# Kernel optimization log

Hardware: AMD Instinct MI355X
Metric: run time of the kernel (lower is better)

The kernel has to match this reference:

```python
import jax, jax.numpy as jnp
import numpy as np

NUM_GRAPHS = 64


def setup_inputs() -> dict:
    key = jax.random.key(0)
    ks = jax.random.split(key, 8)
    N, E, D_IN, D_H = 50000, 800000, 128, 256
    x = jax.random.uniform(ks[0], (N, D_IN), dtype=jnp.float32)
    edge_index = jax.random.randint(ks[1], (2, E), 0, N, dtype=jnp.int64)
    batch = jnp.sort(jax.random.randint(ks[2], (N,), 0, NUM_GRAPHS, dtype=jnp.int64))
    s = 1.0 / np.sqrt(D_IN)
    s2 = 1.0 / np.sqrt(D_H)
    W1_rel = jax.random.normal(ks[3], (D_IN, D_H), dtype=jnp.float32) * s
    W1_root = jax.random.normal(ks[4], (D_IN, D_H), dtype=jnp.float32) * s
    b1 = jnp.zeros((D_H,), jnp.float32)
    W2_rel = jax.random.normal(ks[5], (D_H, D_H), dtype=jnp.float32) * s2
    W2_root = jax.random.normal(ks[6], (D_H, D_H), dtype=jnp.float32) * s2
    b2 = jnp.zeros((D_H,), jnp.float32)
    return {"x": x, "edge_index": edge_index, "batch": batch,
            "W1_rel": W1_rel, "W1_root": W1_root, "b1": b1,
            "W2_rel": W2_rel, "W2_root": W2_root, "b2": b2}


def reference(x, edge_index, batch, W1_rel, W1_root, b1, W2_rel, W2_root, b2):
    N = x.shape[0]
    src, dst = edge_index[0], edge_index[1]

    # handcrafted features: per-label fraction of total feature mass + log(graph_size)
    graph_size = jnp.sum(x)
    handcrafted = jnp.concatenate([jnp.sum(x, axis=0) / graph_size,
                                   jnp.log(graph_size)[None]])

    def graph_conv(h, W_rel, W_root, b):
        # PyG GraphConv (aggr='add'): out_i = W_rel @ sum_{j->i} h_j + W_root @ h_i + b
        agg = jax.ops.segment_sum(h[src], dst, num_segments=N)  # [N, d]
        return agg @ W_rel + h @ W_root + b

    h = jax.nn.relu(graph_conv(x, W1_rel, W1_root, b1))
    # layers 2..num_layers share the same weights (module instance reused in original)
    for _ in range(2):
        h = jax.nn.relu(graph_conv(h, W2_rel, W2_root, b2))

    # global_mean_pool over batch ids
    counts = jax.ops.segment_sum(jnp.ones((N,), h.dtype), batch, num_segments=NUM_GRAPHS)
    pooled = jax.ops.segment_sum(h, batch, num_segments=NUM_GRAPHS)
    pooled = pooled / jnp.maximum(counts, 1.0)[:, None]
    return pooled, handcrafted
```

## Files before the change

kernel.cpp:

```cpp
#include <hip/hip_runtime.h>
#include <hip/hip_bf16.h>
#include <string.h>

#define NN 50000
#define NE 800000
#define DIN 128
#define DH 256
#define NG 64
#define PSPLIT 32

typedef short bf16x8 __attribute__((ext_vector_type(8)));
typedef float f32x4 __attribute__((ext_vector_type(4)));

__device__ __forceinline__ float bf2f(__hip_bfloat16 v) { return __bfloat162float(v); }
__device__ __forceinline__ float bfbits(unsigned int lo16) {
  unsigned int u = lo16 << 16;
  float f;
  memcpy(&f, &u, 4);
  return f;
}
__device__ __forceinline__ unsigned int packbf2(float x, float y) {
  __hip_bfloat16 bx = __float2bfloat16(x), by = __float2bfloat16(y);
  unsigned short ux, uy;
  memcpy(&ux, &bx, 2);
  memcpy(&uy, &by, 2);
  return (unsigned int)ux | ((unsigned int)uy << 16);
}

__device__ __forceinline__ float loadF(const void* p, long i, int fbf) {
  return fbf ? bf2f(((const __hip_bfloat16*)p)[i]) : ((const float*)p)[i];
}
__device__ __forceinline__ void storeF(void* p, long i, float v, int fbf) {
  if (fbf) ((__hip_bfloat16*)p)[i] = __float2bfloat16(v);
  else ((float*)p)[i] = v;
}
__device__ __forceinline__ int loadI(const void* p, long i, int i64) {
  return i64 ? (int)((const long long*)p)[i] : ((const int*)p)[i];
}

__global__ void k_detect(const void* x, const void* ei, int* flags) {
  __shared__ int s_f32sig, s_i32sig;
  if (threadIdx.x == 0) { s_f32sig = 0; s_i32sig = 0; }
  __syncthreads();
  int t = threadIdx.x;
  const unsigned short* u = (const unsigned short*)x;
  int f = 0;
  for (int i = 2 * t; i < 8192; i += 512) if (u[i] >= 0x4000) f = 1;
  const unsigned int* w = (const unsigned int*)ei;
  int g = 0;
  for (int i = 2 * t + 1; i < 8192; i += 512) if (w[i] != 0u) g = 1;
  if (f) atomicOr(&s_f32sig, 1);
  if (g) atomicOr(&s_i32sig, 1);
  __syncthreads();
  if (t == 0) { flags[0] = s_f32sig ? 0 : 1; flags[1] = s_i32sig ? 0 : 1; }
}

__global__ void k_zero(int* __restrict__ p, int n) {
  int i = blockIdx.x * blockDim.x + threadIdx.x;
  int stride = gridDim.x * blockDim.x;
  for (; i < n; i += stride) p[i] = 0;
}

__global__ __launch_bounds__(256) void k_prep(
    const void* __restrict__ x, __hip_bfloat16* __restrict__ xb,
    float* __restrict__ colsum, const int* __restrict__ flags) {
  int fbf = flags[0];
  int t = threadIdx.x;
  int lane16 = t & 15;
  int rowoff = t >> 4;
  float acc[8] = {};
  for (int r = blockIdx.x * 16 + rowoff; r < NN; r += gridDim.x * 16) {
    uint4 o;
    if (fbf) {
      uint4 v = ((const uint4*)x)[(long)r * 16 + lane16];
      acc[0] += bfbits(v.x & 0xffffu); acc[1] += bfbits(v.x >> 16);
      acc[2] += bfbits(v.y & 0xffffu); acc[3] += bfbits(v.y >> 16);
      acc[4] += bfbits(v.z & 0xffffu); acc[5] += bfbits(v.z >> 16);
      acc[6] += bfbits(v.w & 0xffffu); acc[7] += bfbits(v.w >> 16);
      o = v;
    } else {
      float4 a = ((const float4*)x)[(long)r * 32 + lane16 * 2];
      float4 b = ((const float4*)x)[(long)r * 32 + lane16 * 2 + 1];
      acc[0] += a.x; acc[1] += a.y; acc[2] += a.z; acc[3] += a.w;
      acc[4] += b.x; acc[5] += b.y; acc[6] += b.z; acc[7] += b.w;
      o.x = packbf2(a.x, a.y); o.y = packbf2(a.z, a.w);
      o.z = packbf2(b.x, b.y); o.w = packbf2(b.z, b.w);
    }
    ((uint4*)xb)[(long)r * 16 + lane16] = o;
  }
  __shared__ float s[16][DIN];
#pragma unroll
  for (int k = 0; k < 8; ++k) s[rowoff][lane16 * 8 + k] = acc[k];
  __syncthreads();
  if (t < DIN) {
    float v = 0.f;
#pragma unroll
    for (int ro = 0; ro < 16; ++ro) v += s[ro][t];
    atomicAdd(&colsum[t], v);
  }
}

__global__ void k_handcrafted(const float* __restrict__ colsum, void* __restrict__ out,
                              const int* __restrict__ flags) {
  __shared__ float s[DIN];
  int fbf = flags[0];
  int t = threadIdx.x;
  s[t] = colsum[t];
  __syncthreads();
  for (int off = DIN / 2; off > 0; off >>= 1) {
    if (t < off) s[t] += s[t + off];
    __syncthreads();
  }
  float g = s[0];
  storeF(out, NG * DH + t, colsum[t] / g, fbf);
  if (t == 0) storeF(out, NG * DH + DIN, logf(g), fbf);
}

__global__ void k_pack_w(const void* __restrict__ Wrel, const void* __restrict__ Wroot,
                         const void* __restrict__ bias, __hip_bfloat16* __restrict__ pack,
                         float* __restrict__ biasf, const int* __restrict__ flags, int K) {
  int fbf = flags[0];
  int KS = K >> 5;
  int total = 2 * K * DH;
  int i = blockIdx.x * blockDim.x + threadIdx.x;
  int stride = gridDim.x * blockDim.x;
  for (int p = i; p < total; p += stride) {
    int m = p / (K * DH);
    int r = p % (K * DH);
    int j = r & 7;
    int l = (r >> 3) & 63;
    int q2 = r >> 9;
    int ks = q2 % KS;
    int ct = q2 / KS;
    int kk = ks * 32 + (l >> 4) * 8 + j;
    int col = ct * 16 + (l & 15);
    const void* W = m ? Wroot : Wrel;
    pack[p] = __float2bfloat16(loadF(W, (long)kk * DH + col, fbf));
  }
  if (i < DH) biasf[i] = loadF(bias, i, fbf);
}

__global__ void k_deg(const void* __restrict__ ei, int* __restrict__ cnt,
                      const int* __restrict__ flags) {
  int i64 = flags[1];
  int e = blockIdx.x * blockDim.x + threadIdx.x;
  int stride = gridDim.x * blockDim.x;
  for (; e < NE; e += stride) {
    int d = loadI(ei, (long)NE + e, i64);
    d = min(max(d, 0), NN - 1);
    atomicAdd(&cnt[d], 1);
  }
}

#define SCAN_B 256
__global__ void k_scan1(const int* __restrict__ cnt, int* __restrict__ rowptr,
                        int* __restrict__ bsum) {
  __shared__ int s[SCAN_B];
  int b = blockIdx.x, t = threadIdx.x;
  int i = b * SCAN_B + t;
  int v = (i < NN) ? cnt[i] : 0;
  s[t] = v;
  __syncthreads();
  for (int off = 1; off < SCAN_B; off <<= 1) {
    int xv = (t >= off) ? s[t - off] : 0;
    __syncthreads();
    s[t] += xv;
    __syncthreads();
  }
  if (i < NN) rowptr[i] = s[t] - v;
  if (t == SCAN_B - 1) bsum[b] = s[t];
}

__global__ void k_scan2(int* __restrict__ bsum, int nb) {
  __shared__ int s[SCAN_B];
  int t = threadIdx.x;
  int v = (t < nb) ? bsum[t] : 0;
  s[t] = v;
  __syncthreads();
  for (int off = 1; off < SCAN_B; off <<= 1) {
    int xv = (t >= off) ? s[t - off] : 0;
    __syncthreads();
    s[t] += xv;
    __syncthreads();
  }
  if (t < nb) bsum[t] = s[t] - v;
}

__global__ void k_scan3(int* __restrict__ rowptr, const int* __restrict__ bsum) {
  int i = blockIdx.x * blockDim.x + threadIdx.x;
  int stride = gridDim.x * blockDim.x;
  for (; i < NN; i += stride) rowptr[i] += bsum[i >> 8];
  if (blockIdx.x == 0 && threadIdx.x == 0) rowptr[NN] = NE;
}

__global__ void k_fill(const void* __restrict__ ei, const int* __restrict__ rowptr,
                       int* __restrict__ cur, int* __restrict__ srcs,
                       const int* __restrict__ flags) {
  int i64 = flags[1];
  int e = blockIdx.x * blockDim.x + threadIdx.x;
  int stride = gridDim.x * blockDim.x;
  for (; e < NE; e += stride) {
    int s = loadI(ei, e, i64);
    int d = loadI(ei, (long)NE + e, i64);
    s = min(max(s, 0), NN - 1);
    d = min(max(d, 0), NN - 1);
    int p = atomicAdd(&cur[d], 1);
    srcs[rowptr[d] + p] = s;
  }
}

__global__ __launch_bounds__(256) void k_gather256(
    const int* __restrict__ rowptr, const int* __restrict__ srcs,
    const __hip_bfloat16* __restrict__ h, __hip_bfloat16* __restrict__ agg) {
  int node = blockIdx.x * 4 + (threadIdx.x >> 6);
  if (node >= NN) return;
  int lane = threadIdx.x & 63;
  int beg = rowptr[node], end = rowptr[node + 1];
  const uint2* h2 = (const uint2*)h;
  float a0 = 0.f, a1 = 0.f, a2 = 0.f, a3 = 0.f;
  int i = beg;
  for (; i + 7 < end; i += 8) {
    uint2 v[8];
#pragma unroll
    for (int u = 0; u < 8; ++u) v[u] = h2[srcs[i + u] * 64 + lane];
#pragma unroll
    for (int u = 0; u < 8; ++u) {
      a0 += bfbits(v[u].x & 0xffffu);
      a1 += bfbits(v[u].x >> 16);
      a2 += bfbits(v[u].y & 0xffffu);
      a3 += bfbits(v[u].y >> 16);
    }
  }
  for (; i < end; ++i) {
    uint2 v0 = h2[srcs[i] * 64 + lane];
    a0 += bfbits(v0.x & 0xffffu);
    a1 += bfbits(v0.x >> 16);
    a2 += bfbits(v0.y & 0xffffu);
    a3 += bfbits(v0.y >> 16);
  }
  uint2 o;
  o.x = packbf2(a0, a1);
  o.y = packbf2(a2, a3);
  ((uint2*)agg)[node * 64 + lane] = o;
}

__global__ __launch_bounds__(256) void k_gather128(
    const int* __restrict__ rowptr, const int* __restrict__ srcs,
    const __hip_bfloat16* __restrict__ h, __hip_bfloat16* __restrict__ agg) {
  int node = blockIdx.x * 4 + (threadIdx.x >> 6);
  if (node >= NN) return;
  int lane = threadIdx.x & 63;
  int beg = rowptr[node], end = rowptr[node + 1];
  const unsigned int* h2 = (const unsigned int*)h;
  float a0 = 0.f, a1 = 0.f;
  int i = beg;
  for (; i + 7 < end; i += 8) {
    unsigned int v[8];
#pragma unroll
    for (int u = 0; u < 8; ++u) v[u] = h2[srcs[i + u] * 64 + lane];
#pragma unroll
    for (int u = 0; u < 8; ++u) {
      a0 += bfbits(v[u] & 0xffffu);
      a1 += bfbits(v[u] >> 16);
    }
  }
  for (; i < end; ++i) {
    unsigned int v0 = h2[srcs[i] * 64 + lane];
    a0 += bfbits(v0 & 0xffffu);
    a1 += bfbits(v0 >> 16);
  }
  ((unsigned int*)agg)[node * 64 + lane] = packbf2(a0, a1);
}

template <int K>
__global__ __launch_bounds__(256, 4) void k_gemm(
    const __hip_bfloat16* __restrict__ A1, const __hip_bfloat16* __restrict__ A2,
    const __hip_bfloat16* __restrict__ Wpack, const float* __restrict__ bias,
    __hip_bfloat16* __restrict__ out) {
  constexpr int KS = K >> 5;
  int lane = threadIdx.x & 63;
  int wave = threadIdx.x >> 6;
  int m15 = lane & 15;
  int q = lane >> 4;
  int row0 = blockIdx.x * 32;
  const short* A1s = (const short*)A1;
  const short* A2s = (const short*)A2;
  const short* Wp = (const short*)Wpack;
  const int wrootOfs = K * DH;
  f32x4 acc[2][4] = {};
#pragma unroll
  for (int ks = 0; ks < KS; ++ks) {
    int kofs = ks * 32 + q * 8;
    bf16x8 a1[2], a2[2], b1[4], b2[4];
#pragma unroll
    for (int mt = 0; mt < 2; ++mt) {
      int r = row0 + mt * 16 + m15;
      if (r > NN - 1) r = NN - 1;
      a1[mt] = *(const bf16x8*)(A1s + r * K + kofs);
      a2[mt] = *(const bf16x8*)(A2s + r * K + kofs);
    }
#pragma unroll
    for (int ct = 0; ct < 4; ++ct) {
      int gct = wave * 4 + ct;
      const short* base = Wp + ((gct * KS + ks) * 64 + lane) * 8;
      b1[ct] = *(const bf16x8*)(base);
      b2[ct] = *(const bf16x8*)(base + wrootOfs);
    }
#pragma unroll
    for (int mt = 0; mt < 2; ++mt)
#pragma unroll
      for (int ct = 0; ct < 4; ++ct) {
        acc[mt][ct] = __builtin_amdgcn_mfma_f32_16x16x32_bf16(a1[mt], b1[ct], acc[mt][ct], 0, 0, 0);
        acc[mt][ct] = __builtin_amdgcn_mfma_f32_16x16x32_bf16(a2[mt], b2[ct], acc[mt][ct], 0, 0, 0);
      }
  }
#pragma unroll
  for (int mt = 0; mt < 2; ++mt)
#pragma unroll
    for (int ct = 0; ct < 4; ++ct) {
      int col = (wave * 4 + ct) * 16 + m15;
      float bv = bias[col];
#pragma unroll
      for (int r = 0; r < 4; ++r) {
        int row = row0 + mt * 16 + q * 4 + r;
        if (row < NN) {
          float v = acc[mt][ct][r] + bv;
          out[row * DH + col] = __float2bfloat16(fmaxf(v, 0.f));
        }
      }
    }
}

__global__ void k_bounds(const void* __restrict__ batch, int* __restrict__ gstart,
                         int* __restrict__ gend, const int* __restrict__ flags) {
  int i64 = flags[1];
  int n = blockIdx.x * blockDim.x + threadIdx.x;
  if (n >= NN) return;
  int b = min(max(loadI(batch, n, i64), 0), NG - 1);
  int bp = (n == 0) ? -1 : min(max(loadI(batch, n - 1, i64), 0), NG - 1);
  if (b != bp) gstart[b] = n;
  int bn = (n == NN - 1) ? -1 : min(max(loadI(batch, n + 1, i64), 0), NG - 1);
  if (b != bn) gend[b] = n + 1;
}

__global__ void k_poolpart(const int* __restrict__ gstart, const int* __restrict__ gend,
                           const __hip_bfloat16* __restrict__ h, float* __restrict__ pooled) {
  int g = blockIdx.x;
  int p = blockIdx.y;
  int j = threadIdx.x;
  int s = gstart[g], e = gend[g];
  int len = e - s;
  if (len <= 0) return;
  int chunk = (len + PSPLIT - 1) / PSPLIT;
  int rs = s + p * chunk;
  int re = min(rs + chunk, e);
  if (rs >= re) return;
  const unsigned int* h2 = (const unsigned int*)h;
  float a0 = 0.f, a1 = 0.f;
  for (int r = rs; r < re; ++r) {
    unsigned int v = h2[(long)r * 128 + j];
    a0 += bfbits(v & 0xffffu);
    a1 += bfbits(v >> 16);
  }
  atomicAdd(&pooled[g * DH + 2 * j], a0);
  atomicAdd(&pooled[g * DH + 2 * j + 1], a1);
}

__global__ void k_poolfin(const int* __restrict__ gstart, const int* __restrict__ gend,
                          const float* __restrict__ pooled, void* __restrict__ out,
                          const int* __restrict__ flags) {
  int fbf = flags[0];
  int g = blockIdx.x;
  int j = threadIdx.x;
  float cnt = fmaxf((float)(gend[g] - gstart[g]), 1.0f);
  storeF(out, (long)g * DH + j, pooled[g * DH + j] / cnt, fbf);
}

extern "C" void kernel_launch(void* const* d_in, const int* in_sizes, int n_in,
                              void* d_out, int out_size, void* d_ws, size_t ws_size,
                              hipStream_t stream) {
  const void* x = d_in[0];
  const void* ei = d_in[1];
  const void* batch = d_in[2];
  const void* W1r = d_in[3];
  const void* W1o = d_in[4];
  const void* b1 = d_in[5];
  const void* W2r = d_in[6];
  const void* W2o = d_in[7];
  const void* b2 = d_in[8];
  void* out = d_out;

  char* w = (char*)d_ws;
  auto alloc = [&](size_t bytes) -> char* {
    char* p = w;
    w += (bytes + 255) & ~(size_t)255;
    return p;
  };
  int* flags = (int*)alloc(64);
  const int zero_n = NN + NN + DIN + NG + NG + NG * DH;
  int* zreg = (int*)alloc((size_t)zero_n * 4);
  int* cnt = zreg;
  int* cur = cnt + NN;
  float* colsum = (float*)(cur + NN);
  int* gstart = (int*)(colsum + DIN);
  int* gend = gstart + NG;
  float* pooled = (float*)(gend + NG);
  int* rowptr = (int*)alloc((NN + 1) * 4);
  int* bsum = (int*)alloc(SCAN_B * 4);
  int* srcs = (int*)alloc((size_t)NE * 4);
  __hip_bfloat16* xb = (__hip_bfloat16*)alloc((size_t)NN * DIN * 2);
  __hip_bfloat16* aggb = (__hip_bfloat16*)alloc((size_t)NN * DH * 2);
  __hip_bfloat16* hA = (__hip_bfloat16*)alloc((size_t)NN * DH * 2);
  __hip_bfloat16* hB = (__hip_bfloat16*)alloc((size_t)NN * DH * 2);
  __hip_bfloat16* wp1 = (__hip_bfloat16*)alloc((size_t)2 * DIN * DH * 2);
  __hip_bfloat16* wp2 = (__hip_bfloat16*)alloc((size_t)2 * DH * DH * 2);
  float* b1f = (float*)alloc(DH * 4);
  float* b2f = (float*)alloc(DH * 4);

  const int nblk = (NN + SCAN_B - 1) / SCAN_B;
  const int gemm_grid = (NN + 31) / 32;
  const int gat_grid = (NN + 3) / 4;

  k_detect<<<1, 256, 0, stream>>>(x, ei, flags);
  k_zero<<<512, 256, 0, stream>>>(zreg, zero_n);

  k_pack_w<<<64, 256, 0, stream>>>(W1r, W1o, b1, wp1, b1f, flags, DIN);
  k_pack_w<<<128, 256, 0, stream>>>(W2r, W2o, b2, wp2, b2f, flags, DH);
  k_prep<<<1024, 256, 0, stream>>>(x, xb, colsum, flags);
  k_handcrafted<<<1, 128, 0, stream>>>(colsum, out, flags);

  k_deg<<<1024, 256, 0, stream>>>(ei, cnt, flags);
  k_scan1<<<nblk, SCAN_B, 0, stream>>>(cnt, rowptr, bsum);
  k_scan2<<<1, SCAN_B, 0, stream>>>(bsum, nblk);
  k_scan3<<<256, 256, 0, stream>>>(rowptr, bsum);
  k_fill<<<1024, 256, 0, stream>>>(ei, rowptr, cur, srcs, flags);

  k_gather128<<<gat_grid, 256, 0, stream>>>(rowptr, srcs, xb, aggb);
  k_gemm<DIN><<<gemm_grid, 256, 0, stream>>>(aggb, xb, wp1, b1f, hA);
  k_gather256<<<gat_grid, 256, 0, stream>>>(rowptr, srcs, hA, aggb);
  k_gemm<DH><<<gemm_grid, 256, 0, stream>>>(aggb, hA, wp2, b2f, hB);
  k_gather256<<<gat_grid, 256, 0, stream>>>(rowptr, srcs, hB, aggb);
  k_gemm<DH><<<gemm_grid, 256, 0, stream>>>(aggb, hB, wp2, b2f, hA);

  k_bounds<<<nblk, 256, 0, stream>>>(batch, gstart, gend, flags);
  k_poolpart<<<dim3(NG, PSPLIT), 128, 0, stream>>>(gstart, gend, hA, pooled);
  k_poolfin<<<NG, DH, 0, stream>>>(gstart, gend, pooled, out, flags);
}
```

Measured before the change: 499.6 us.

## Split gather kernels into column slices with edge-parallel lanes per node

The neighbor-gather kernels now split the feature columns into 8 slices handled by separate blocks, with block id low bits selecting the slice. Within a wave, lane groups process different edges of the same node in parallel and are combined with shuffle reductions. The aim is a smaller per-pass working set of h that fits better in cache, plus more memory-level parallelism per node. Edge index loads and agg stores use nontemporal hints. In exchange, the srcs lists and rowptr are re-read 8 times and each 4-byte load is narrow and scattered.

```diff
diff --git a/kernel.cpp b/kernel.cpp
--- a/kernel.cpp
+++ b/kernel.cpp
@@ -209,67 +209,93 @@
   }
 }
 
-__global__ __launch_bounds__(256) void k_gather256(
+#define GNB ((NN + 15) / 16)
+
+__global__ __launch_bounds__(256) void k_gather256x(
     const int* __restrict__ rowptr, const int* __restrict__ srcs,
     const __hip_bfloat16* __restrict__ h, __hip_bfloat16* __restrict__ agg) {
-  int node = blockIdx.x * 4 + (threadIdx.x >> 6);
-  if (node >= NN) return;
+  int bid = blockIdx.x;
+  int s = bid & 7;
+  int nb = bid >> 3;
+  int wave = threadIdx.x >> 6;
   int lane = threadIdx.x & 63;
-  int beg = rowptr[node], end = rowptr[node + 1];
-  const uint2* h2 = (const uint2*)h;
-  float a0 = 0.f, a1 = 0.f, a2 = 0.f, a3 = 0.f;
-  int i = beg;
-  for (; i + 7 < end; i += 8) {
-    uint2 v[8];
-#pragma unroll
-    for (int u = 0; u < 8; ++u) v[u] = h2[srcs[i + u] * 64 + lane];
-#pragma unroll
-    for (int u = 0; u < 8; ++u) {
-      a0 += bfbits(v[u].x & 0xffffu);
-      a1 += bfbits(v[u].x >> 16);
-      a2 += bfbits(v[u].y & 0xffffu);
-      a3 += bfbits(v[u].y >> 16);
-    }
-  }
-  for (; i < end; ++i) {
-    uint2 v0 = h2[srcs[i] * 64 + lane];
-    a0 += bfbits(v0.x & 0xffffu);
-    a1 += bfbits(v0.x >> 16);
-    a2 += bfbits(v0.y & 0xffffu);
-    a3 += bfbits(v0.y >> 16);
-  }
-  uint2 o;
-  o.x = packbf2(a0, a1);
-  o.y = packbf2(a2, a3);
-  ((uint2*)agg)[node * 64 + lane] = o;
-}
-
-__global__ __launch_bounds__(256) void k_gather128(
+  int g = lane >> 4;
+  int c = lane & 15;
+  const unsigned int* h2 = (const unsigned int*)h;
+  unsigned int* agg2 = (unsigned int*)agg;
+  int colofs = s * 16 + c;
+#pragma unroll
+  for (int nw = 0; nw < 4; ++nw) {
+    int node = nb * 16 + wave * 4 + nw;
+    if (node >= NN) break;
+    int beg = rowptr[node], end = rowptr[node + 1];
+    float a0 = 0.f, a1 = 0.f;
+    int i = beg + g;
+    for (; i + 12 < end; i += 16) {
+      int s0 = __builtin_nontemporal_load(&srcs[i]);
+      int s1 = __builtin_nontemporal_load(&srcs[i + 4]);
+      int s2 = __builtin_nontemporal_load(&srcs[i + 8]);
+      int s3 = __builtin_nontemporal_load(&srcs[i + 12]);
+      unsigned v0 = h2[(long)s0 * 128 + colofs];
+      unsigned v1 = h2[(long)s1 * 128 + colofs];
+      unsigned v2 = h2[(long)s2 * 128 + colofs];
+      unsigned v3 = h2[(long)s3 * 128 + colofs];
+      a0 += bfbits(v0 & 0xffffu) + bfbits(v1 & 0xffffu) +
+            bfbits(v2 & 0xffffu) + bfbits(v3 & 0xffffu);
+      a1 += bfbits(v0 >> 16) + bfbits(v1 >> 16) + bfbits(v2 >> 16) + bfbits(v3 >> 16);
+    }
+    for (; i < end; i += 4) {
+      int s0 = __builtin_nontemporal_load(&srcs[i]);
+      unsigned v0 = h2[(long)s0 * 128 + colofs];
+      a0 += bfbits(v0 & 0xffffu);
+      a1 += bfbits(v0 >> 16);
+    }
+    a0 += __shfl_xor(a0, 16); a0 += __shfl_xor(a0, 32);
+    a1 += __shfl_xor(a1, 16); a1 += __shfl_xor(a1, 32);
+    if (g == 0)
+      __builtin_nontemporal_store(packbf2(a0, a1), &agg2[(long)node * 128 + colofs]);
+  }
+}
+
+__global__ __launch_bounds__(256) void k_gather128x(
     const int* __restrict__ rowptr, const int* __restrict__ srcs,
     const __hip_bfloat16* __restrict__ h, __hip_bfloat16* __restrict__ agg) {
-  int node = blockIdx.x * 4 + (threadIdx.x >> 6);
-  if (node >= NN) return;
+  int bid = blockIdx.x;
+  int s = bid & 7;
+  int nb = bid >> 3;
+  int wave = threadIdx.x >> 6;
   int lane = threadIdx.x & 63;
-  int beg = rowptr[node], end = rowptr[node + 1];
+  int g = lane >> 3;
+  int c = lane & 7;
   const unsigned int* h2 = (const unsigned int*)h;
-  float a0 = 0.f, a1 = 0.f;
-  int i = beg;
-  for (; i + 7 < end; i += 8) {
-    unsigned int v[8];
-#pragma unroll
-    for (int u = 0; u < 8; ++u) v[u] = h2[srcs[i + u] * 64 + lane];
-#pragma unroll
-    for (int u = 0; u < 8; ++u) {
-      a0 += bfbits(v[u] & 0xffffu);
-      a1 += bfbits(v[u] >> 16);
-    }
-  }
-  for (; i < end; ++i) {
-    unsigned int v0 = h2[srcs[i] * 64 + lane];
-    a0 += bfbits(v0 & 0xffffu);
-    a1 += bfbits(v0 >> 16);
-  }
-  ((unsigned int*)agg)[node * 64 + lane] = packbf2(a0, a1);
+  unsigned int* agg2 = (unsigned int*)agg;
+  int colofs = s * 8 + c;
+#pragma unroll
+  for (int nw = 0; nw < 4; ++nw) {
+    int node = nb * 16 + wave * 4 + nw;
+    if (node >= NN) break;
+    int beg = rowptr[node], end = rowptr[node + 1];
+    float a0 = 0.f, a1 = 0.f;
+    int i = beg + g;
+    for (; i + 8 < end; i += 16) {
+      int s0 = __builtin_nontemporal_load(&srcs[i]);
+      int s1 = __builtin_nontemporal_load(&srcs[i + 8]);
+      unsigned v0 = h2[(long)s0 * 64 + colofs];
+      unsigned v1 = h2[(long)s1 * 64 + colofs];
+      a0 += bfbits(v0 & 0xffffu) + bfbits(v1 & 0xffffu);
+      a1 += bfbits(v0 >> 16) + bfbits(v1 >> 16);
+    }
+    for (; i < end; i += 8) {
+      int s0 = __builtin_nontemporal_load(&srcs[i]);
+      unsigned v0 = h2[(long)s0 * 64 + colofs];
+      a0 += bfbits(v0 & 0xffffu);
+      a1 += bfbits(v0 >> 16);
+    }
+    a0 += __shfl_xor(a0, 8); a0 += __shfl_xor(a0, 16); a0 += __shfl_xor(a0, 32);
+    a1 += __shfl_xor(a1, 8); a1 += __shfl_xor(a1, 16); a1 += __shfl_xor(a1, 32);
+    if (g == 0)
+      __builtin_nontemporal_store(packbf2(a0, a1), &agg2[(long)node * 64 + colofs]);
+  }
 }
 
 template <int K>
@@ -419,7 +445,7 @@
 
   const int nblk = (NN + SCAN_B - 1) / SCAN_B;
   const int gemm_grid = (NN + 31) / 32;
-  const int gat_grid = (NN + 3) / 4;
+  const int gat_grid = 8 * GNB;
 
   k_detect<<<1, 256, 0, stream>>>(x, ei, flags);
   k_zero<<<512, 256, 0, stream>>>(zreg, zero_n);
@@ -435,11 +461,11 @@
   k_scan3<<<256, 256, 0, stream>>>(rowptr, bsum);
   k_fill<<<1024, 256, 0, stream>>>(ei, rowptr, cur, srcs, flags);
 
-  k_gather128<<<gat_grid, 256, 0, stream>>>(rowptr, srcs, xb, aggb);
+  k_gather128x<<<gat_grid, 256, 0, stream>>>(rowptr, srcs, xb, aggb);
   k_gemm<DIN><<<gemm_grid, 256, 0, stream>>>(aggb, xb, wp1, b1f, hA);
-  k_gather256<<<gat_grid, 256, 0, stream>>>(rowptr, srcs, hA, aggb);
+  k_gather256x<<<gat_grid, 256, 0, stream>>>(rowptr, srcs, hA, aggb);
   k_gemm<DH><<<gemm_grid, 256, 0, stream>>>(aggb, hA, wp2, b2f, hB);
-  k_gather256<<<gat_grid, 256, 0, stream>>>(rowptr, srcs, hB, aggb);
+  k_gather256x<<<gat_grid, 256, 0, stream>>>(rowptr, srcs, hB, aggb);
   k_gemm<DH><<<gemm_grid, 256, 0, stream>>>(aggb, hB, wp2, b2f, hA);
 
   k_bounds<<<nblk, 256, 0, stream>>>(batch, gstart, gend, flags);
```

Result: slower. 900.7 us (+80.3%).

## Store node features in column-sliced layout so gathers read from L2-sized slices

Applied to the files above, without the earlier changes.

Node feature matrices (input x and hidden layers 1-2) are now stored as 32-column slices, each a contiguous [N,32] array, written by the prep and GEMM epilogues. The gather kernel is rewritten so each block handles one slice for a range of nodes. Eight lane-groups per wave split a node's edges and are combined with shuffle reductions, and srcs loads and agg stores use nontemporal hints. The aim is to keep each slice's random-access working set resident in cache during the gather, at the cost of re-reading the CSR index once per slice and a strided write pattern in the GEMM epilogue.

```diff
diff --git a/kernel.cpp b/kernel.cpp
--- a/kernel.cpp
+++ b/kernel.cpp
@@ -11,6 +11,7 @@
 
 typedef short bf16x8 __attribute__((ext_vector_type(8)));
 typedef float f32x4 __attribute__((ext_vector_type(4)));
+typedef unsigned int u32x2 __attribute__((ext_vector_type(2)));
 
 __device__ __forceinline__ float bf2f(__hip_bfloat16 v) { return __bfloat162float(v); }
 __device__ __forceinline__ float bfbits(unsigned int lo16) {
@@ -62,7 +63,7 @@
 }
 
 __global__ __launch_bounds__(256) void k_prep(
-    const void* __restrict__ x, __hip_bfloat16* __restrict__ xb,
+    const void* __restrict__ x, __hip_bfloat16* __restrict__ xs,
     float* __restrict__ colsum, const int* __restrict__ flags) {
   int fbf = flags[0];
   int t = threadIdx.x;
@@ -86,7 +87,7 @@
       o.x = packbf2(a.x, a.y); o.y = packbf2(a.z, a.w);
       o.z = packbf2(b.x, b.y); o.w = packbf2(b.z, b.w);
     }
-    ((uint4*)xb)[(long)r * 16 + lane16] = o;
+    ((uint4*)xs)[((long)(lane16 >> 2) * NN + r) * 4 + (lane16 & 3)] = o;
   }
   __shared__ float s[16][DIN];
 #pragma unroll
@@ -209,70 +210,66 @@
   }
 }
 
-__global__ __launch_bounds__(256) void k_gather256(
+template <int K>
+__global__ __launch_bounds__(256) void k_gathers(
     const int* __restrict__ rowptr, const int* __restrict__ srcs,
-    const __hip_bfloat16* __restrict__ h, __hip_bfloat16* __restrict__ agg) {
-  int node = blockIdx.x * 4 + (threadIdx.x >> 6);
-  if (node >= NN) return;
+    const __hip_bfloat16* __restrict__ hs, __hip_bfloat16* __restrict__ agg) {
+  constexpr int SL = K / 32;
+  constexpr int HALVES = 8 / SL;
+  constexpr int NPH = (NN + HALVES - 1) / HALVES;
+  int role = blockIdx.x & 7;
+  int nb = blockIdx.x >> 3;
+  int s = role / HALVES;
+  int half = role % HALVES;
+  int wave = threadIdx.x >> 6;
   int lane = threadIdx.x & 63;
-  int beg = rowptr[node], end = rowptr[node + 1];
-  const uint2* h2 = (const uint2*)h;
-  float a0 = 0.f, a1 = 0.f, a2 = 0.f, a3 = 0.f;
-  int i = beg;
-  for (; i + 7 < end; i += 8) {
-    uint2 v[8];
-#pragma unroll
-    for (int u = 0; u < 8; ++u) v[u] = h2[srcs[i + u] * 64 + lane];
-#pragma unroll
-    for (int u = 0; u < 8; ++u) {
-      a0 += bfbits(v[u].x & 0xffffu);
-      a1 += bfbits(v[u].x >> 16);
-      a2 += bfbits(v[u].y & 0xffffu);
-      a3 += bfbits(v[u].y >> 16);
-    }
-  }
-  for (; i < end; ++i) {
-    uint2 v0 = h2[srcs[i] * 64 + lane];
-    a0 += bfbits(v0.x & 0xffffu);
-    a1 += bfbits(v0.x >> 16);
-    a2 += bfbits(v0.y & 0xffffu);
-    a3 += bfbits(v0.y >> 16);
-  }
-  uint2 o;
-  o.x = packbf2(a0, a1);
-  o.y = packbf2(a2, a3);
-  ((uint2*)agg)[node * 64 + lane] = o;
-}
-
-__global__ __launch_bounds__(256) void k_gather128(
-    const int* __restrict__ rowptr, const int* __restrict__ srcs,
-    const __hip_bfloat16* __restrict__ h, __hip_bfloat16* __restrict__ agg) {
-  int node = blockIdx.x * 4 + (threadIdx.x >> 6);
-  if (node >= NN) return;
-  int lane = threadIdx.x & 63;
-  int beg = rowptr[node], end = rowptr[node + 1];
-  const unsigned int* h2 = (const unsigned int*)h;
-  float a0 = 0.f, a1 = 0.f;
-  int i = beg;
-  for (; i + 7 < end; i += 8) {
-    unsigned int v[8];
-#pragma unroll
-    for (int u = 0; u < 8; ++u) v[u] = h2[srcs[i + u] * 64 + lane];
-#pragma unroll
-    for (int u = 0; u < 8; ++u) {
-      a0 += bfbits(v[u] & 0xffffu);
-      a1 += bfbits(v[u] >> 16);
-    }
-  }
-  for (; i < end; ++i) {
-    unsigned int v0 = h2[srcs[i] * 64 + lane];
-    a0 += bfbits(v0 & 0xffffu);
-    a1 += bfbits(v0 >> 16);
-  }
-  ((unsigned int*)agg)[node * 64 + lane] = packbf2(a0, a1);
-}
-
-template <int K>
+  int g = lane >> 3;
+  int c = lane & 7;
+  const u32x2* h2 = (const u32x2*)hs;
+  u32x2* agg2 = (u32x2*)agg;
+  long sbase = (long)s * NN;
+  int nlim = min((half + 1) * NPH, NN);
+#pragma unroll
+  for (int nw = 0; nw < 4; ++nw) {
+    int node = half * NPH + nb * 16 + wave * 4 + nw;
+    if (node >= nlim) break;
+    int beg = rowptr[node], end = rowptr[node + 1];
+    float a0 = 0.f, a1 = 0.f, a2 = 0.f, a3 = 0.f;
+    int i = beg + g;
+    for (; i + 8 < end; i += 16) {
+      int s0 = __builtin_nontemporal_load(&srcs[i]);
+      int s1 = __builtin_nontemporal_load(&srcs[i + 8]);
+      u32x2 v0 = h2[(sbase + s0) * 8 + c];
+      u32x2 v1 = h2[(sbase + s1) * 8 + c];
+      a0 += bfbits(v0.x & 0xffffu) + bfbits(v1.x & 0xffffu);
+      a1 += bfbits(v0.x >> 16) + bfbits(v1.x >> 16);
+      a2 += bfbits(v0.y & 0xffffu) + bfbits(v1.y & 0xffffu);
+      a3 += bfbits(v0.y >> 16) + bfbits(v1.y >> 16);
+    }
+    for (; i < end; i += 8) {
+      int s0 = __builtin_nontemporal_load(&srcs[i]);
+      u32x2 v0 = h2[(sbase + s0) * 8 + c];
+      a0 += bfbits(v0.x & 0xffffu);
+      a1 += bfbits(v0.x >> 16);
+      a2 += bfbits(v0.y & 0xffffu);
+      a3 += bfbits(v0.y >> 16);
+    }
+    a0 += __shfl_xor(a0, 8); a1 += __shfl_xor(a1, 8);
+    a2 += __shfl_xor(a2, 8); a3 += __shfl_xor(a3, 8);
+    a0 += __shfl_xor(a0, 16); a1 += __shfl_xor(a1, 16);
+    a2 += __shfl_xor(a2, 16); a3 += __shfl_xor(a3, 16);
+    a0 += __shfl_xor(a0, 32); a1 += __shfl_xor(a1, 32);
+    a2 += __shfl_xor(a2, 32); a3 += __shfl_xor(a3, 32);
+    if (g == 0) {
+      u32x2 o;
+      o.x = packbf2(a0, a1);
+      o.y = packbf2(a2, a3);
+      __builtin_nontemporal_store(o, &agg2[(long)node * (K / 4) + s * 8 + c]);
+    }
+  }
+}
+
+template <int K, bool OUTS>
 __global__ __launch_bounds__(256, 4) void k_gemm(
     const __hip_bfloat16* __restrict__ A1, const __hip_bfloat16* __restrict__ A2,
     const __hip_bfloat16* __restrict__ Wpack, const float* __restrict__ bias,
@@ -296,8 +293,8 @@
     for (int mt = 0; mt < 2; ++mt) {
       int r = row0 + mt * 16 + m15;
       if (r > NN - 1) r = NN - 1;
-      a1[mt] = *(const bf16x8*)(A1s + r * K + kofs);
-      a2[mt] = *(const bf16x8*)(A2s + r * K + kofs);
+      a1[mt] = *(const bf16x8*)(A1s + (long)r * K + kofs);
+      a2[mt] = *(const bf16x8*)(A2s + ((long)ks * NN + r) * 32 + q * 8);
     }
 #pragma unroll
     for (int ct = 0; ct < 4; ++ct) {
@@ -325,7 +322,9 @@
         int row = row0 + mt * 16 + q * 4 + r;
         if (row < NN) {
           float v = acc[mt][ct][r] + bv;
-          out[row * DH + col] = __float2bfloat16(fmaxf(v, 0.f));
+          long oidx = OUTS ? (((long)(col >> 5) * NN + row) * 32 + (col & 31))
+                           : ((long)row * DH + col);
+          out[oidx] = __float2bfloat16(fmaxf(v, 0.f));
         }
       }
     }
@@ -408,25 +407,27 @@
   int* rowptr = (int*)alloc((NN + 1) * 4);
   int* bsum = (int*)alloc(SCAN_B * 4);
   int* srcs = (int*)alloc((size_t)NE * 4);
-  __hip_bfloat16* xb = (__hip_bfloat16*)alloc((size_t)NN * DIN * 2);
+  __hip_bfloat16* xs = (__hip_bfloat16*)alloc((size_t)NN * DIN * 2);
   __hip_bfloat16* aggb = (__hip_bfloat16*)alloc((size_t)NN * DH * 2);
-  __hip_bfloat16* hA = (__hip_bfloat16*)alloc((size_t)NN * DH * 2);
-  __hip_bfloat16* hB = (__hip_bfloat16*)alloc((size_t)NN * DH * 2);
+  __hip_bfloat16* h1s = (__hip_bfloat16*)alloc((size_t)NN * DH * 2);
+  __hip_bfloat16* h2s = (__hip_bfloat16*)alloc((size_t)NN * DH * 2);
   __hip_bfloat16* wp1 = (__hip_bfloat16*)alloc((size_t)2 * DIN * DH * 2);
   __hip_bfloat16* wp2 = (__hip_bfloat16*)alloc((size_t)2 * DH * DH * 2);
   float* b1f = (float*)alloc(DH * 4);
   float* b2f = (float*)alloc(DH * 4);
+  __hip_bfloat16* hA = h1s;
 
   const int nblk = (NN + SCAN_B - 1) / SCAN_B;
   const int gemm_grid = (NN + 31) / 32;
-  const int gat_grid = (NN + 3) / 4;
+  const int g256_grid = 8 * ((NN + 15) / 16);
+  const int g128_grid = 8 * ((NN / 2 + 15) / 16);
 
   k_detect<<<1, 256, 0, stream>>>(x, ei, flags);
   k_zero<<<512, 256, 0, stream>>>(zreg, zero_n);
 
   k_pack_w<<<64, 256, 0, stream>>>(W1r, W1o, b1, wp1, b1f, flags, DIN);
   k_pack_w<<<128, 256, 0, stream>>>(W2r, W2o, b2, wp2, b2f, flags, DH);
-  k_prep<<<1024, 256, 0, stream>>>(x, xb, colsum, flags);
+  k_prep<<<1024, 256, 0, stream>>>(x, xs, colsum, flags);
   k_handcrafted<<<1, 128, 0, stream>>>(colsum, out, flags);
 
   k_deg<<<1024, 256, 0, stream>>>(ei, cnt, flags);
@@ -435,12 +436,12 @@
   k_scan3<<<256, 256, 0, stream>>>(rowptr, bsum);
   k_fill<<<1024, 256, 0, stream>>>(ei, rowptr, cur, srcs, flags);
 
-  k_gather128<<<gat_grid, 256, 0, stream>>>(rowptr, srcs, xb, aggb);
-  k_gemm<DIN><<<gemm_grid, 256, 0, stream>>>(aggb, xb, wp1, b1f, hA);
-  k_gather256<<<gat_grid, 256, 0, stream>>>(rowptr, srcs, hA, aggb);
-  k_gemm<DH><<<gemm_grid, 256, 0, stream>>>(aggb, hA, wp2, b2f, hB);
-  k_gather256<<<gat_grid, 256, 0, stream>>>(rowptr, srcs, hB, aggb);
-  k_gemm<DH><<<gemm_grid, 256, 0, stream>>>(aggb, hB, wp2, b2f, hA);
+  k_gathers<DIN><<<g128_grid, 256, 0, stream>>>(rowptr, srcs, xs, aggb);
+  k_gemm<DIN, true><<<gemm_grid, 256, 0, stream>>>(aggb, xs, wp1, b1f, h1s);
+  k_gathers<DH><<<g256_grid, 256, 0, stream>>>(rowptr, srcs, h1s, aggb);
+  k_gemm<DH, true><<<gemm_grid, 256, 0, stream>>>(aggb, h1s, wp2, b2f, h2s);
+  k_gathers<DH><<<g256_grid, 256, 0, stream>>>(rowptr, srcs, h2s, aggb);
+  k_gemm<DH, false><<<gemm_grid, 256, 0, stream>>>(aggb, h2s, wp2, b2f, hA);
 
   k_bounds<<<nblk, 256, 0, stream>>>(batch, gstart, gend, flags);
   k_poolpart<<<dim3(NG, PSPLIT), 128, 0, stream>>>(gstart, gend, hA, pooled);
```

After: 679.7 us. 1.36x slower.
